# Optimization experiments

Hardware: AMD Instinct MI355X
Metric: run time of the kernel (lower is better)

The kernel has to match this reference:

```python
import jax, jax.numpy as jnp
import numpy as np

B, SQ, SKV, D = 4, 2048, 2048, 2048
NEG = -1e9


def setup_inputs() -> dict:
    key = jax.random.key(0)
    ks = jax.random.split(key, 7)
    x = jax.random.normal(ks[0], (B, SKV, D), dtype=jnp.float32)
    enc_q = jax.random.normal(ks[1], (B, SQ, D), dtype=jnp.float32)
    enc_k = jax.random.normal(ks[2], (B, SKV, D), dtype=jnp.float32)
    i_mask = jax.random.bernoulli(ks[3], 0.1, (B, SQ, SKV))  # True -> masked
    s = 1.0 / np.sqrt(D)
    Wq = jax.random.normal(ks[4], (D, D), dtype=jnp.float32) * s
    Wk = jax.random.normal(ks[5], (D, D), dtype=jnp.float32) * s
    Wv = jax.random.normal(ks[6], (D, D), dtype=jnp.float32) * s
    return {"x": x, "enc_q": enc_q, "enc_k": enc_k, "i_mask": i_mask,
            "Wq": Wq, "Wk": Wk, "Wv": Wv}


def reference(x, enc_q, enc_k, i_mask, Wq, Wk, Wv):
    # Bias-free linear projections (nn.Linear: y = x @ W^T)
    q = jnp.einsum('bsd,ed->bse', enc_q, Wq)   # [B,SQ,D]
    k = jnp.einsum('bsd,ed->bse', enc_k, Wk)   # [B,SKV,D]
    v = jnp.einsum('bsd,ed->bse', x, Wv)       # [B,SKV,D]
    scale = 1.0 / jnp.sqrt(jnp.asarray(q.shape[-1], q.dtype))
    scores = jnp.einsum('bqd,bkd->bqk', q, k) * scale  # [B,SQ,SKV]
    scores = jnp.where(i_mask, jnp.asarray(NEG, scores.dtype), scores)
    attn = jax.nn.softmax(scores, axis=-1)
    return jnp.einsum('bqk,bkd->bqd', attn, v)  # [B,SQ,D]
```

## Files before the change

### kernel.cpp

```cpp
#include <hip/hip_runtime.h>
#include <stdint.h>

typedef short  short8  __attribute__((ext_vector_type(8)));
typedef unsigned short ushort8 __attribute__((ext_vector_type(8)));
typedef unsigned short ushort4v __attribute__((ext_vector_type(4)));
typedef float  f32x4   __attribute__((ext_vector_type(4)));

#define BB  4
#define SQL 2048
#define SKL 2048
#define NEGV -1e9f
#define AS1 __attribute__((address_space(1)))
#define AS3 __attribute__((address_space(3)))

__device__ __forceinline__ unsigned short f2bf(float f){
  union { float f; uint32_t u; } x; x.f = f;
  return (unsigned short)((x.u + 0x7FFFu + ((x.u >> 16) & 1u)) >> 16);
}
__device__ __forceinline__ float bf2f(unsigned short h){
  union { uint32_t u; float f; } x; x.u = ((uint32_t)h) << 16;
  return x.f;
}

#define BARR() __builtin_amdgcn_s_barrier()
#define LGKM0() asm volatile("s_waitcnt lgkmcnt(0)" ::: "memory")
#define VMW(N)  asm volatile("s_waitcnt vmcnt(" #N ")"   ::: "memory")
#define PRIO1 __builtin_amdgcn_s_setprio(1)
#define PRIO0 __builtin_amdgcn_s_setprio(0)

__global__ void mask_detect(const uint8_t* __restrict__ m, int* __restrict__ cnt){
  const long n4 = (long)BB * SQL * SKL / 4;
  long idx  = (long)blockIdx.x * blockDim.x + threadIdx.x;
  long step = (long)gridDim.x * blockDim.x;
  int c0 = 0, c1 = 0, c2 = 0;
  for (long i4 = idx; i4 < n4; i4 += step){
    uchar4 b = ((const uchar4*)m)[i4];
    c0 += (b.y != 0) + (b.z != 0) + (b.w != 0);
    c1 += (b.x > 1) + (b.y > 1) + (b.z > 1) + (b.w > 1);
    c2 += (b.y != 0);
  }
  #pragma unroll
  for (int o = 32; o >= 1; o >>= 1){
    c0 += __shfl_xor(c0, o); c1 += __shfl_xor(c1, o); c2 += __shfl_xor(c2, o);
  }
  if ((threadIdx.x & 63) == 0){
    atomicAdd(&cnt[0], c0); atomicAdd(&cnt[1], c1); atomicAdd(&cnt[2], c2);
  }
}

__global__ __launch_bounds__(256)
void prep(const float* __restrict__ s0, const float* __restrict__ s1,
          const float* __restrict__ s2, const float* __restrict__ s3,
          unsigned short* __restrict__ d0, unsigned short* __restrict__ d1,
          unsigned short* __restrict__ d2, unsigned short* __restrict__ d3,
          const float* __restrict__ tq, const float* __restrict__ tk,
          unsigned short* __restrict__ dq, unsigned short* __restrict__ dk)
{
  if (blockIdx.x < 2048){
    const long total = 6815744;
    for (long c = (long)blockIdx.x * 256 + threadIdx.x; c < total; c += 2048 * 256){
      const float* s; unsigned short* d; long off;
      if      (c < 2097152){ s = s0; d = d0; off = c; }
      else if (c < 4194304){ s = s1; d = d1; off = c - 2097152; }
      else if (c < 6291456){ s = s2; d = d2; off = c - 4194304; }
      else                 { s = s3; d = d3; off = c - 6291456; }
      f32x4 a = ((const f32x4*)s)[off * 2];
      f32x4 b = ((const f32x4*)s)[off * 2 + 1];
      ushort8 w;
      #pragma unroll
      for (int j = 0; j < 4; ++j){ w[j] = f2bf(a[j]); w[j + 4] = f2bf(b[j]); }
      ((ushort8*)d)[off] = w;
    }
  } else {
    __shared__ float t[32][33];
    const int j = blockIdx.x - 2048;
    const int z = j >> 12, rem = j & 4095;
    const float* s = z ? tk : tq;
    unsigned short* d = z ? dk : dq;
    const long bx = (long)(rem & 63) * 32, by = (long)(rem >> 6) * 32;
    const int tx = threadIdx.x & 31, ty = threadIdx.x >> 5;
    #pragma unroll
    for (int jj = 0; jj < 4; ++jj)
      t[ty + jj * 8][tx] = s[(by + ty + jj * 8) * 2048 + bx + tx];
    __syncthreads();
    #pragma unroll
    for (int jj = 0; jj < 4; ++jj)
      d[(bx + ty + jj * 8) * 2048 + by + tx] = f2bf(t[tx][ty + jj * 8]);
  }
}

__device__ __forceinline__ void xcd_decode(int& bx, int& by, int& bz){
  const int gx = gridDim.x, gy = gridDim.y;
  const int nwg = gx * gy * gridDim.z;
  const int lid = blockIdx.x + gx * (blockIdx.y + gy * blockIdx.z);
  const int sw  = (lid & 7) * (nwg >> 3) + (lid >> 3);
  bx = sw % gx;
  const int t = sw / gx;
  by = t % gy;
  bz = t / gy;
}

template<int EPI>
__device__ __forceinline__ void gemm256_body(
    const unsigned short* __restrict__ Ag, const unsigned short* __restrict__ Bg,
    void* __restrict__ Cb, int bz, long Cbs, long tm, long tn, float scale,
    unsigned short (&lA)[2][16384], unsigned short (&lB)[2][16384])
{
  constexpr int LD = 2048;
  const int tid = threadIdx.x, lane = tid & 63, wid = tid >> 6;
  const int wm = wid >> 2, wn = wid & 3;
  const int l15 = lane & 15, l16 = lane >> 4;

  f32x4 acc[2][2][4][2] = {};
  short8 aF[4][2];
  short8 bF[2][2][2];

  auto stageA = [&](int buf, int half, int k){
    const unsigned short* s = Ag + (tm + half * 128) * LD + k;
    unsigned short* d = lA[buf] + half * 8192;
    #pragma unroll
    for (int l = 0; l < 2; ++l){
      const int idx = l * 512 + tid;
      const int r   = idx >> 3;
      const int gsw = (idx & 7) ^ (r & 7);
      __builtin_amdgcn_global_load_lds((const AS1 void*)(s + r * LD + gsw * 8),
                                       (AS3 void*)(d + idx * 8), 16, 0, 0);
    }
  };
  auto stageB = [&](int buf, int half, int k){
    const unsigned short* s = Bg + (tn + half * 128) * LD + k;
    unsigned short* d = lB[buf] + half * 8192;
    #pragma unroll
    for (int l = 0; l < 2; ++l){
      const int idx = l * 512 + tid;
      const int r   = idx >> 3;
      const int gsw = (idx & 7) ^ (r & 7);
      __builtin_amdgcn_global_load_lds((const AS1 void*)(s + r * LD + gsw * 8),
                                       (AS3 void*)(d + idx * 8), 16, 0, 0);
    }
  };

  #define RD_A(BUF, QM)                                                       \
    _Pragma("unroll")                                                         \
    for (int mr = 0; mr < 4; ++mr)                                            \
      _Pragma("unroll")                                                       \
      for (int ks = 0; ks < 2; ++ks){                                         \
        const int r = (QM) * 128 + wm * 64 + mr * 16 + l15;                   \
        const int g = ks * 4 + l16;                                           \
        aF[mr][ks] = *(const short8*)&lA[(BUF)][(r * 8 + (g ^ (r & 7))) * 8]; \
      }
  #define RD_B(BUF, QN)                                                       \
    _Pragma("unroll")                                                         \
    for (int nr = 0; nr < 2; ++nr)                                            \
      _Pragma("unroll")                                                       \
      for (int ks = 0; ks < 2; ++ks){                                         \
        const int c = (QN) * 128 + wn * 32 + nr * 16 + l15;                   \
        const int g = ks * 4 + l16;                                           \
        bF[QN][nr][ks] = *(const short8*)&lB[(BUF)][(c * 8 + (g ^ (c & 7))) * 8]; \
      }
  #define MFMA16(QM, QN)                                                      \
    _Pragma("unroll")                                                         \
    for (int mr = 0; mr < 4; ++mr)                                            \
      _Pragma("unroll")                                                       \
      for (int nr = 0; nr < 2; ++nr)                                          \
        _Pragma("unroll")                                                     \
        for (int ks = 0; ks < 2; ++ks)                                        \
          acc[QM][QN][mr][nr] = __builtin_amdgcn_mfma_f32_16x16x32_bf16(      \
              aF[mr][ks], bF[QN][nr][ks], acc[QM][QN][mr][nr], 0, 0, 0);

  #define KTILE_MAIN(BUF, KNXT)                                               \
  {                                                                           \
    RD_A(BUF, 0); RD_B(BUF, 0);                                               \
    stageA((BUF) ^ 1, 0, (KNXT));                                             \
    BARR(); LGKM0();                                                          \
    PRIO1; MFMA16(0, 0); PRIO0; VMW(4); BARR();                               \
    RD_B(BUF, 1);                                                             \
    stageB((BUF) ^ 1, 0, (KNXT));                                             \
    BARR(); LGKM0();                                                          \
    PRIO1; MFMA16(0, 1); PRIO0; VMW(4); BARR();                               \
    RD_A(BUF, 1);                                                             \
    stageB((BUF) ^ 1, 1, (KNXT));                                             \
    BARR(); LGKM0();                                                          \
    PRIO1; MFMA16(1, 1); PRIO0; BARR();                                       \
    stageA((BUF) ^ 1, 1, (KNXT));                                             \
    BARR();                                                                   \
    PRIO1; MFMA16(1, 0); PRIO0; VMW(2); BARR();                               \
  }
  #define KTILE_LAST(BUF)                                                     \
  {                                                                           \
    RD_A(BUF, 0); RD_B(BUF, 0);                                               \
    BARR(); LGKM0();                                                          \
    PRIO1; MFMA16(0, 0); PRIO0; VMW(2); BARR();                               \
    RD_B(BUF, 1);                                                             \
    BARR(); LGKM0();                                                          \
    PRIO1; MFMA16(0, 1); PRIO0; VMW(0); BARR();                               \
    RD_A(BUF, 1);                                                             \
    BARR(); LGKM0();                                                          \
    PRIO1; MFMA16(1, 1); PRIO0; BARR();                                       \
    PRIO1; MFMA16(1, 0); PRIO0;                                               \
  }

  stageA(0, 0, 0);
  stageB(0, 0, 0);
  stageB(0, 1, 0);
  stageA(0, 1, 0);
  VMW(4); BARR();

  for (int it = 0; it < 15; ++it){
    KTILE_MAIN(0, (2 * it + 1) * 64);
    KTILE_MAIN(1, (2 * it + 2) * 64);
  }
  KTILE_MAIN(0, 31 * 64);
  KTILE_LAST(1);

  const int colo = l15, rowg = l16 * 4;
  if constexpr (EPI == 0){
    unsigned short* C = (unsigned short*)Cb + (long)bz * Cbs;
    #pragma unroll
    for (int qm = 0; qm < 2; ++qm)
      #pragma unroll
      for (int qn = 0; qn < 2; ++qn)
        #pragma unroll
        for (int mr = 0; mr < 4; ++mr)
          #pragma unroll
          for (int j = 0; j < 4; ++j){
            const long row = tm + qm * 128 + wm * 64 + mr * 16 + rowg + j;
            unsigned short* cr = C + row * LD + tn + qn * 128 + wn * 32 + colo;
            #pragma unroll
            for (int nr = 0; nr < 2; ++nr) cr[nr * 16] = f2bf(acc[qm][qn][mr][nr][j] * scale);
          }
  } else {
    float* C = (float*)Cb + (long)bz * Cbs;
    #pragma unroll
    for (int qm = 0; qm < 2; ++qm)
      #pragma unroll
      for (int qn = 0; qn < 2; ++qn)
        #pragma unroll
        for (int mr = 0; mr < 4; ++mr)
          #pragma unroll
          for (int j = 0; j < 4; ++j){
            const long row = tm + qm * 128 + wm * 64 + mr * 16 + rowg + j;
            float* cr = C + row * LD + tn + qn * 128 + wn * 32 + colo;
            #pragma unroll
            for (int nr = 0; nr < 2; ++nr) cr[nr * 16] = acc[qm][qn][mr][nr][j];
          }
  }
  #undef RD_A
  #undef RD_B
  #undef MFMA16
  #undef KTILE_MAIN
  #undef KTILE_LAST
}

template<int EPI>
__global__ __launch_bounds__(512, 2)
void gemm256(const unsigned short* __restrict__ A, const unsigned short* __restrict__ B,
             void* __restrict__ Cb, long Abs, long Bbs, long Cbs, float scale)
{
  __shared__ unsigned short lA[2][16384];
  __shared__ unsigned short lB[2][16384];
  int bx, by, bz; xcd_decode(bx, by, bz);
  gemm256_body<EPI>(A + (long)bz * Abs, B + (long)bz * Bbs, Cb, bz, Cbs,
                    (long)by * 256, (long)bx * 256, scale, lA, lB);
}

__global__ __launch_bounds__(512, 2)
void gemm256_proj2(const unsigned short* A0, const unsigned short* A1,
                   const unsigned short* B0, const unsigned short* B1,
                   void* C0, void* C1)
{
  __shared__ unsigned short lA[2][16384];
  __shared__ unsigned short lB[2][16384];
  int bx, by, bz; xcd_decode(bx, by, bz);
  const int sec = bz >> 2, b = bz & 3;
  const long NN = (long)SQL * 2048;
  const unsigned short* Av = sec ? A1 : A0;
  const unsigned short* Bv = sec ? B1 : B0;
  void*                 Cv = sec ? C1 : C0;
  const long Abs = sec ? 0 : NN;
  const long Bbs = sec ? NN : 0;
  gemm256_body<0>(Av + (long)b * Abs, Bv + (long)b * Bbs, Cv, b, NN,
                  (long)by * 256, (long)bx * 256, 1.f, lA, lB);
}

template<int AMODE, int BMODE, int EPI>
__device__ __forceinline__ void gemm_body(
    const void* __restrict__ Av, const void* __restrict__ Bv,
    void* __restrict__ Cb, int bz, long Abs, long Bbs, long Cbs,
    long tm, long tn, float scale, int koff, int klen,
    unsigned short (*lA)[4096], unsigned short (*lB)[4096])
{
  constexpr int LD = 2048;
  const int tid = threadIdx.x, lane = tid & 63, wave = tid >> 6;
  const int wr = wave >> 1, wc = wave & 1;
  const int c0 = tid, c1 = tid + 256;
  const int r0 = c0 >> 2, q0 = (c0 & 3) * 8;
  const int r1 = c1 >> 2, q1 = (c1 & 3) * 8;

  const unsigned short* A16 = (const unsigned short*)Av + (long)bz * Abs;
  const unsigned short* B16 = (const unsigned short*)Bv + (long)bz * Bbs;
  const float*          A32 = (const float*)Av + (long)bz * Abs;
  const float*          B32 = (const float*)Bv + (long)bz * Bbs;

  f32x4 acc[4][4] = {};
  f32x4 sA[4], sB[4];

  auto issueA = [&](int buf, int kk){
    if constexpr (AMODE == 0){
      __builtin_amdgcn_global_load_lds((const AS1 void*)(A16 + (tm + r0) * LD + q0 + kk),
                                       (AS3 void*)(lA[buf] + c0 * 8), 16, 0, 0);
      __builtin_amdgcn_global_load_lds((const AS1 void*)(A16 + (tm + r1) * LD + q1 + kk),
                                       (AS3 void*)(lA[buf] + c1 * 8), 16, 0, 0);
    } else {
      sA[0] = *(const f32x4*)(A32 + (tm + r0) * LD + q0 + kk);
      sA[1] = *(const f32x4*)(A32 + (tm + r0) * LD + q0 + kk + 4);
      sA[2] = *(const f32x4*)(A32 + (tm + r1) * LD + q1 + kk);
      sA[3] = *(const f32x4*)(A32 + (tm + r1) * LD + q1 + kk + 4);
    }
  };
  auto issueB = [&](int buf, int kk){
    if constexpr (BMODE == 0){
      __builtin_amdgcn_global_load_lds((const AS1 void*)(B16 + (tn + r0) * LD + q0 + kk),
                                       (AS3 void*)(lB[buf] + c0 * 8), 16, 0, 0);
      __builtin_amdgcn_global_load_lds((const AS1 void*)(B16 + (tn + r1) * LD + q1 + kk),
                                       (AS3 void*)(lB[buf] + c1 * 8), 16, 0, 0);
    } else {
      sB[0] = *(const f32x4*)(B32 + (tn + r0) * LD + q0 + kk);
      sB[1] = *(const f32x4*)(B32 + (tn + r0) * LD + q0 + kk + 4);
      sB[2] = *(const f32x4*)(B32 + (tn + r1) * LD + q1 + kk);
      sB[3] = *(const f32x4*)(B32 + (tn + r1) * LD + q1 + kk + 4);
    }
  };
  auto writeA = [&](int buf){
    if constexpr (AMODE == 1){
      ushort8 w0, w1;
      #pragma unroll
      for (int j = 0; j < 4; ++j){
        w0[j] = f2bf(sA[0][j]); w0[j + 4] = f2bf(sA[1][j]);
        w1[j] = f2bf(sA[2][j]); w1[j + 4] = f2bf(sA[3][j]);
      }
      *(ushort8*)(lA[buf] + c0 * 8) = w0;
      *(ushort8*)(lA[buf] + c1 * 8) = w1;
    }
  };
  auto writeB = [&](int buf){
    if constexpr (BMODE == 1){
      ushort8 w0, w1;
      #pragma unroll
      for (int j = 0; j < 4; ++j){
        w0[j] = f2bf(sB[0][j]); w0[j + 4] = f2bf(sB[1][j]);
        w1[j] = f2bf(sB[2][j]); w1[j + 4] = f2bf(sB[3][j]);
      }
      *(ushort8*)(lB[buf] + c0 * 8) = w0;
      *(ushort8*)(lB[buf] + c1 * 8) = w1;
    }
  };
  auto computeTile = [&](int buf){
    short8 aF[4], bF[4];
    #pragma unroll
    for (int m = 0; m < 4; ++m)
      aF[m] = *(const short8*)(lA[buf] + (wr * 64 + m * 16 + (lane & 15)) * 32 + (lane >> 4) * 8);
    #pragma unroll
    for (int n = 0; n < 4; ++n)
      bF[n] = *(const short8*)(lB[buf] + (wc * 64 + n * 16 + (lane & 15)) * 32 + (lane >> 4) * 8);
    #pragma unroll
    for (int m = 0; m < 4; ++m)
      #pragma unroll
      for (int n = 0; n < 4; ++n)
        acc[m][n] = __builtin_amdgcn_mfma_f32_16x16x32_bf16(aF[m], bF[n], acc[m][n], 0, 0, 0);
  };

  issueA(0, koff); issueB(0, koff); writeA(0); writeB(0);
  __syncthreads();
  int cur = 0;
  for (int k0 = koff; k0 < koff + klen - 32; k0 += 32){
    issueA(cur ^ 1, k0 + 32);
    issueB(cur ^ 1, k0 + 32);
    computeTile(cur);
    writeA(cur ^ 1); writeB(cur ^ 1);
    __syncthreads();
    cur ^= 1;
  }
  computeTile(cur);

  const int colo = lane & 15, rowg = (lane >> 4) * 4;
  if constexpr (EPI == 0){
    unsigned short* C = (unsigned short*)Cb + (long)bz * Cbs;
    #pragma unroll
    for (int m = 0; m < 4; ++m)
      #pragma unroll
      for (int j = 0; j < 4; ++j){
        const long row = tm + wr * 64 + m * 16 + rowg + j;
        unsigned short* cr = C + row * LD + tn + wc * 64 + colo;
        #pragma unroll
        for (int n = 0; n < 4; ++n) cr[n * 16] = f2bf(acc[m][n][j] * scale);
      }
  } else {
    float* C = (float*)Cb + (long)bz * Cbs;
    #pragma unroll
    for (int m = 0; m < 4; ++m)
      #pragma unroll
      for (int j = 0; j < 4; ++j){
        const long row = tm + wr * 64 + m * 16 + rowg + j;
        float* cr = C + row * LD + tn + wc * 64 + colo;
        #pragma unroll
        for (int n = 0; n < 4; ++n) cr[n * 16] = acc[m][n][j];
      }
  }
}

template<int AMODE, int BMODE, int EPI>
__global__ __launch_bounds__(256, 2)
void gemm_nt(const void* __restrict__ Abv, const void* __restrict__ Bbv,
             void* __restrict__ Cb, long Abs, long Bbs, long Cbs, float scale)
{
  __shared__ unsigned short lA[2][4096];
  __shared__ unsigned short lB[2][4096];
  int bx, by, bz; xcd_decode(bx, by, bz);
  gemm_body<AMODE, BMODE, EPI>(Abv, Bbv, Cb, bz, Abs, Bbs, Cbs,
                               (long)by * 128, (long)bx * 128, scale, 0, 2048, lA, lB);
}

__global__ __launch_bounds__(256, 2)
void gemm_splitk(const unsigned short* __restrict__ A, const unsigned short* __restrict__ B,
                 float* __restrict__ Cp)
{
  __shared__ unsigned short lA[2][4096];
  __shared__ unsigned short lB[2][4096];
  int bx, by, bz; xcd_decode(bx, by, bz);
  gemm_body<0, 0, 2>(A, B, Cp + (long)bz * 4194304, 0, 0, 0, 4194304,
                     (long)by * 128, (long)bx * 128, 1.f, bz * 512, 512, lA, lB);
}

__global__ __launch_bounds__(256)
void mt_reduce(const float* __restrict__ Cp, unsigned short* __restrict__ Mt, float scale){
  for (long c = (long)blockIdx.x * blockDim.x + threadIdx.x; c < 1048576;
       c += (long)gridDim.x * blockDim.x){
    f32x4 a = ((const f32x4*)Cp)[c];
    f32x4 b = ((const f32x4*)(Cp + 4194304))[c];
    f32x4 d = ((const f32x4*)(Cp + 8388608))[c];
    f32x4 e = ((const f32x4*)(Cp + 12582912))[c];
    ushort4v w;
    #pragma unroll
    for (int j = 0; j < 4; ++j) w[j] = f2bf((a[j] + b[j] + d[j] + e[j]) * scale);
    ((ushort4v*)Mt)[c] = w;
  }
}

__global__ __launch_bounds__(256, 2)
void gemm_proj3f(const void* A0, const void* A1, const void* A2,
                 const void* B0, const void* B1, const void* B2,
                 void* C0, void* C1, void* C2)
{
  __shared__ unsigned short lA[2][4096];
  __shared__ unsigned short lB[2][4096];
  int bx, by, bz; xcd_decode(bx, by, bz);
  const int sec = bz >> 2, b = bz & 3;
  const long NN = (long)SQL * 2048;
  const void* Av = sec == 0 ? A0 : sec == 1 ? A1 : A2;
  const void* Bv = sec == 0 ? B0 : sec == 1 ? B1 : B2;
  void*       Cv = sec == 0 ? C0 : sec == 1 ? C1 : C2;
  const long Abs = (sec == 2) ? 0 : NN;
  const long Bbs = (sec == 2) ? NN : 0;
  gemm_body<1, 1, 0>(Av, Bv, Cv, b, Abs, Bbs, NN,
                     (long)by * 128, (long)bx * 128, 1.f, 0, 2048, lA, lB);
}

__global__ __launch_bounds__(256, 4)
void softmax_rows(const unsigned short* __restrict__ S, const void* __restrict__ mask,
                  const int* __restrict__ cnt, unsigned short* __restrict__ P){
  const long row = blockIdx.x;
  const int t = threadIdx.x;
  const int a0 = cnt[0], a1 = cnt[1], a2 = cnt[2];
  const int mmode = (a1 == 0) ? (a0 > 1000 ? 0 : 1) : (a2 > 1000 ? 2 : 3);

  ushort8 u = *((const ushort8*)(S + row * SKL) + t);
  float v[8];
  #pragma unroll
  for (int j = 0; j < 8; ++j) v[j] = bf2f(u[j]);

  const long mb = row * SKL + (long)t * 8;
  if (mmode == 0){
    uchar4 m0 = ((const uchar4*)mask)[mb / 4], m1 = ((const uchar4*)mask)[mb / 4 + 1];
    if (m0.x) v[0] = NEGV; if (m0.y) v[1] = NEGV; if (m0.z) v[2] = NEGV; if (m0.w) v[3] = NEGV;
    if (m1.x) v[4] = NEGV; if (m1.y) v[5] = NEGV; if (m1.z) v[6] = NEGV; if (m1.w) v[7] = NEGV;
  } else if (mmode == 1){
    int4 m0 = ((const int4*)mask)[mb / 4], m1 = ((const int4*)mask)[mb / 4 + 1];
    if (m0.x) v[0] = NEGV; if (m0.y) v[1] = NEGV; if (m0.z) v[2] = NEGV; if (m0.w) v[3] = NEGV;
    if (m1.x) v[4] = NEGV; if (m1.y) v[5] = NEGV; if (m1.z) v[6] = NEGV; if (m1.w) v[7] = NEGV;
  } else if (mmode == 2){
    ushort8 m = ((const ushort8*)mask)[mb / 8];
    #pragma unroll
    for (int j = 0; j < 8; ++j) if (m[j]) v[j] = NEGV;
  } else {
    f32x4 m0 = ((const f32x4*)mask)[mb / 4], m1 = ((const f32x4*)mask)[mb / 4 + 1];
    #pragma unroll
    for (int j = 0; j < 4; ++j){ if (m0[j] != 0.f) v[j] = NEGV; if (m1[j] != 0.f) v[4 + j] = NEGV; }
  }

  float mx = v[0];
  #pragma unroll
  for (int j = 1; j < 8; ++j) mx = fmaxf(mx, v[j]);
  #pragma unroll
  for (int o = 32; o >= 1; o >>= 1) mx = fmaxf(mx, __shfl_xor(mx, o));
  __shared__ float red[8];
  const int wv = t >> 6, ln = t & 63;
  if (ln == 0) red[wv] = mx;
  __syncthreads();
  mx = fmaxf(fmaxf(red[0], red[1]), fmaxf(red[2], red[3]));
  float e[8], sum = 0.f;
  #pragma unroll
  for (int j = 0; j < 8; ++j){ e[j] = exp2f((v[j] - mx) * 1.4426950408889634f); sum += e[j]; }
  #pragma unroll
  for (int o = 32; o >= 1; o >>= 1) sum += __shfl_xor(sum, o);
  if (ln == 0) red[4 + wv] = sum;
  __syncthreads();
  sum = red[4] + red[5] + red[6] + red[7];
  const float inv = 1.0f / sum;
  ushort8 o8;
  #pragma unroll
  for (int j = 0; j < 8; ++j) o8[j] = f2bf(e[j] * inv);
  *((ushort8*)(P + row * SKL) + t) = o8;
}

extern "C" void kernel_launch(void* const* d_in, const int* in_sizes, int n_in,
                              void* d_out, int out_size, void* d_ws, size_t ws_size,
                              hipStream_t stream)
{
  (void)in_sizes; (void)n_in; (void)out_size;
  const void* x    = d_in[0];
  const void* encq = d_in[1];
  const void* enck = d_in[2];
  const void* imsk = d_in[3];
  const void* Wq   = d_in[4];
  const void* Wk   = d_in[5];
  const void* Wv   = d_in[6];

  uint8_t* ws = (uint8_t*)d_ws;
  int* cnt = (int*)ws;
  const long NN = (long)2048 * 2048;
  const float scale = 0.022097086912079608f;

  hipMemsetAsync(cnt, 0, 4096, stream);
  mask_detect<<<256, 256, 0, stream>>>((const uint8_t*)imsk, cnt);

  const size_t FULL_NEED = 4096 + 4ull * 33554432 + 4ull * 8388608;
  if (ws_size >= FULL_NEED){
    unsigned short* xb  = (unsigned short*)(ws + 4096);
    unsigned short* qb  = xb  + 16777216;
    unsigned short* kb  = qb  + 16777216;
    unsigned short* Wvb = kb  + 16777216;
    unsigned short* WqT = Wvb + 4194304;
    unsigned short* WkT = WqT + 4194304;
    unsigned short* Mt  = WkT + 4194304;
    unsigned short* Vt  = Mt  + 4194304;
    unsigned short* U   = (unsigned short*)d_out;
    unsigned short* S   = U + 16777216;
    unsigned short* P   = qb;

    prep<<<10240, 256, 0, stream>>>((const float*)x, (const float*)encq, (const float*)enck,
                                    (const float*)Wv, xb, qb, kb, Wvb,
                                    (const float*)Wq, (const float*)Wk, WqT, WkT);
    gemm_splitk<<<dim3(16, 16, 4), 256, 0, stream>>>(WkT, WqT, (float*)d_out);
    mt_reduce<<<1024, 256, 0, stream>>>((const float*)d_out, Mt, scale);
    gemm256_proj2<<<dim3(8, 8, 8), 512, 0, stream>>>(qb, Wvb, Mt, xb, U, Vt);
    gemm256<0><<<dim3(8, 8, BB), 512, 0, stream>>>(U, kb, S, NN, NN, NN, 1.f);
    softmax_rows<<<BB * SQL, 256, 0, stream>>>(S, imsk, cnt, P);
    gemm256<2><<<dim3(8, 8, BB), 512, 0, stream>>>(P, Vt, d_out, NN, NN, NN, 1.f);
  } else {
    unsigned short* Q  = (unsigned short*)(ws + 4096);
    unsigned short* Kp = Q  + 16777216;
    unsigned short* Vt = Kp + 16777216;
    unsigned short* P  = Q;
    unsigned short* S;
    const size_t need = 4096 + 4ull * 33554432;
    if (ws_size >= need) S = Vt + 16777216;
    else                 S = (unsigned short*)d_out;

    gemm_proj3f<<<dim3(16, 16, 12), 256, 0, stream>>>(encq, enck, Wv, Wq, Wk, x, Q, Kp, Vt);
    gemm_nt<0, 0, 0><<<dim3(16, 16, BB), 256, 0, stream>>>(Q, Kp, S, NN, NN, NN, scale);
    softmax_rows<<<BB * SQL, 256, 0, stream>>>(S, imsk, cnt, P);
    gemm_nt<0, 0, 2><<<dim3(16, 16, BB), 256, 0, stream>>>(P, Vt, d_out, NN, NN, NN, 1.f);
  }
}
```

Measured before the change: 454.1 us.

## Deepen GEMM K-loop prefetch to stage quarter-tiles two iterations ahead

Restructures the double-buffered GEMM main loop so that most of the next-next K tile's A/B quarter-tiles are written into the current buffer as soon as their fragments have been read to registers, while only one quarter goes to the other buffer. This lengthens the global-load lead time, adds a penultimate-tile variant, and changes the waitcnt/barrier placement. The aim is to hide global memory latency better. The cost is more loads in flight and tighter correctness dependence on the LDS read/overwrite ordering.

```diff
diff --git a/kernel.cpp b/kernel.cpp
--- a/kernel.cpp
+++ b/kernel.cpp
@@ -24,6 +24,7 @@
 
 #define BARR() __builtin_amdgcn_s_barrier()
 #define LGKM0() asm volatile("s_waitcnt lgkmcnt(0)" ::: "memory")
+#define LGKMW(N) asm volatile("s_waitcnt lgkmcnt(" #N ")" ::: "memory")
 #define VMW(N)  asm volatile("s_waitcnt vmcnt(" #N ")"   ::: "memory")
 #define PRIO1 __builtin_amdgcn_s_setprio(1)
 #define PRIO0 __builtin_amdgcn_s_setprio(0)
@@ -168,32 +169,47 @@
           acc[QM][QN][mr][nr] = __builtin_amdgcn_mfma_f32_16x16x32_bf16(      \
               aF[mr][ks], bF[QN][nr][ks], acc[QM][QN][mr][nr], 0, 0, 0);
 
-  #define KTILE_MAIN(BUF, KNXT)                                               \
+  #define KTILE_MAIN(BUF, KN1, KN2)                                           \
   {                                                                           \
     RD_A(BUF, 0); RD_B(BUF, 0);                                               \
-    stageA((BUF) ^ 1, 0, (KNXT));                                             \
+    stageA((BUF) ^ 1, 1, (KN1));                  \
+    LGKMW(8); BARR(); LGKM0();                                                \
+    PRIO1; MFMA16(0, 0); PRIO0; BARR();                                       \
+    RD_B(BUF, 1);                                                             \
+    stageA((BUF), 0, (KN2));                     \
     BARR(); LGKM0();                                                          \
-    PRIO1; MFMA16(0, 0); PRIO0; VMW(4); BARR();                               \
-    RD_B(BUF, 1);                                                             \
-    stageB((BUF) ^ 1, 0, (KNXT));                                             \
-    BARR(); LGKM0();                                                          \
-    PRIO1; MFMA16(0, 1); PRIO0; VMW(4); BARR();                               \
+    PRIO1; MFMA16(0, 1); PRIO0; BARR();                                       \
     RD_A(BUF, 1);                                                             \
-    stageB((BUF) ^ 1, 1, (KNXT));                                             \
+    stageB((BUF), 0, (KN2));                     \
     BARR(); LGKM0();                                                          \
     PRIO1; MFMA16(1, 1); PRIO0; BARR();                                       \
-    stageA((BUF) ^ 1, 1, (KNXT));                                             \
-    BARR();                                                                   \
-    PRIO1; MFMA16(1, 0); PRIO0; VMW(2); BARR();                               \
+    stageB((BUF), 1, (KN2));                     \
+    PRIO1; MFMA16(1, 0); PRIO0;                                               \
+    VMW(6); BARR();                         \
+  }
+  #define KTILE_PEN(BUF, KN1)                                                 \
+  {                                                                           \
+    RD_A(BUF, 0); RD_B(BUF, 0);                                               \
+    stageA((BUF) ^ 1, 1, (KN1));                                              \
+    LGKMW(8); BARR(); LGKM0();                                                \
+    PRIO1; MFMA16(0, 0); PRIO0; BARR();                                       \
+    RD_B(BUF, 1);                                                             \
+    BARR(); LGKM0();                                                          \
+    PRIO1; MFMA16(0, 1); PRIO0; BARR();                                       \
+    RD_A(BUF, 1);                                                             \
+    BARR(); LGKM0();                                                          \
+    PRIO1; MFMA16(1, 1); PRIO0; BARR();                                       \
+    PRIO1; MFMA16(1, 0); PRIO0;                                               \
+    VMW(0); BARR();                                                           \
   }
   #define KTILE_LAST(BUF)                                                     \
   {                                                                           \
     RD_A(BUF, 0); RD_B(BUF, 0);                                               \
     BARR(); LGKM0();                                                          \
-    PRIO1; MFMA16(0, 0); PRIO0; VMW(2); BARR();                               \
+    PRIO1; MFMA16(0, 0); PRIO0; BARR();                                       \
     RD_B(BUF, 1);                                                             \
     BARR(); LGKM0();                                                          \
-    PRIO1; MFMA16(0, 1); PRIO0; VMW(0); BARR();                               \
+    PRIO1; MFMA16(0, 1); PRIO0; BARR();                                       \
     RD_A(BUF, 1);                                                             \
     BARR(); LGKM0();                                                          \
     PRIO1; MFMA16(1, 1); PRIO0; BARR();                                       \
@@ -204,13 +220,16 @@
   stageB(0, 0, 0);
   stageB(0, 1, 0);
   stageA(0, 1, 0);
-  VMW(4); BARR();
+  stageA(1, 0, 64);
+  stageB(1, 0, 64);
+  stageB(1, 1, 64);
+  VMW(6); BARR();
 
   for (int it = 0; it < 15; ++it){
-    KTILE_MAIN(0, (2 * it + 1) * 64);
-    KTILE_MAIN(1, (2 * it + 2) * 64);
-  }
-  KTILE_MAIN(0, 31 * 64);
+    KTILE_MAIN(0, (2 * it + 1) * 64, (2 * it + 2) * 64);
+    KTILE_MAIN(1, (2 * it + 2) * 64, (2 * it + 3) * 64);
+  }
+  KTILE_PEN(0, 31 * 64);
   KTILE_LAST(1);
 
   const int colo = l15, rowg = l16 * 4;
@@ -249,6 +268,7 @@
   #undef RD_B
   #undef MFMA16
   #undef KTILE_MAIN
+  #undef KTILE_PEN
   #undef KTILE_LAST
 }
 
```

New measurement: 452.4 us, median of 3. About the same (-0.4%).
